# Kernel optimization log

Hardware: AMD Instinct MI355X
Metric: run time of the kernel (lower is better)

Reference implementation:

```python
import jax, jax.numpy as jnp
import numpy as np

N = 50000
E = 800000
DIM_IN = 128
DIM_H = 16
HEADS = 8
DIM_OUT = 16
NEG_SLOPE = 0.2


def setup_inputs() -> dict:
    key = jax.random.key(0)
    ks = jax.random.split(key, 12)
    def glorot(k, shape):
        fan_in = shape[0]
        return jax.random.normal(k, shape, dtype=jnp.float32) / np.sqrt(fan_in)
    x = jax.random.normal(ks[0], (N, DIM_IN), dtype=jnp.float32)
    edge_index = jax.random.randint(ks[1], (2, E), 0, N, dtype=jnp.int64)
    # layer 1: GATv2Conv(dim_in, dim_h, heads=8)
    Wl1 = glorot(ks[2], (DIM_IN, HEADS * DIM_H))
    Wr1 = glorot(ks[3], (DIM_IN, HEADS * DIM_H))
    att1 = glorot(ks[4], (HEADS, DIM_H))
    bias1 = jnp.zeros((HEADS * DIM_H,), dtype=jnp.float32)
    # layer 2: GATv2Conv(dim_h*heads, dim_out, heads=1)
    Wl2 = glorot(ks[5], (HEADS * DIM_H, DIM_OUT))
    Wr2 = glorot(ks[6], (HEADS * DIM_H, DIM_OUT))
    att2 = glorot(ks[7], (1, DIM_OUT))
    bias2 = jnp.zeros((DIM_OUT,), dtype=jnp.float32)
    return {"x": x, "edge_index": edge_index, "Wl1": Wl1, "Wr1": Wr1,
            "att1": att1, "bias1": bias1, "Wl2": Wl2, "Wr2": Wr2,
            "att2": att2, "bias2": bias2}


def gatv2_layer(x, src, dst, Wl, Wr, att, bias, n_nodes, heads, ch):
    # x: [N, F_in]; src/dst: [Etot] (self-loops included)
    xl = (x @ Wl).reshape(n_nodes, heads, ch)  # source transform
    xr = (x @ Wr).reshape(n_nodes, heads, ch)  # target transform
    e = jax.nn.leaky_relu(xl[src] + xr[dst], NEG_SLOPE)      # [Etot, H, C]
    logits = jnp.einsum('ehc,hc->eh', e, att)                # [Etot, H]
    # segment softmax over incoming edges of each target node
    m = jax.ops.segment_max(logits, dst, num_segments=n_nodes)
    a = jnp.exp(logits - m[dst])
    denom = jax.ops.segment_sum(a, dst, num_segments=n_nodes)
    alpha = a / denom[dst]                                   # [Etot, H]
    out = jax.ops.segment_sum(xl[src] * alpha[:, :, None], dst,
                              num_segments=n_nodes)          # [N, H, C]
    return out.reshape(n_nodes, heads * ch) + bias


def reference(x, edge_index, Wl1, Wr1, att1, bias1, Wl2, Wr2, att2, bias2):
    # PyG GATv2Conv adds self-loops by default
    loops = jnp.arange(N, dtype=edge_index.dtype)
    src = jnp.concatenate([edge_index[0], loops])
    dst = jnp.concatenate([edge_index[1], loops])
    # dropout is identity in eval mode
    h = gatv2_layer(x, src, dst, Wl1, Wr1, att1, bias1, N, HEADS, DIM_H)
    h = jax.nn.elu(h)
    h = gatv2_layer(h, src, dst, Wl2, Wr2, att2, bias2, N, 1, DIM_OUT)
    return h, jax.nn.log_softmax(h, axis=1)
```

## Files before the change

kernel.cpp:

```cpp
#include <hip/hip_runtime.h>
#include <hip/hip_bf16.h>
#include <math.h>

#define NN 50000
#define EE 800000
#define DIN 128
#define HEADS 8
#define DH 16
#define DOUT 16
#define NEG 0.2f
#define GM 32
#define GB ((NN + GM - 1) / GM)
#define NB ((NN + 255) / 256)
#define DEGB ((EE / 4 + 255) / 256)
#define PAD 64

typedef __attribute__((ext_vector_type(8))) short bf16x8;
typedef __attribute__((ext_vector_type(4))) float f32x4;

__device__ __forceinline__ unsigned pack2bf(float a, float b) {
    union { __hip_bfloat162 h; unsigned u; } c;
    c.h = __float22bfloat162_rn(make_float2(a, b));
    return c.u;
}
__device__ __forceinline__ unsigned short f2bf(float v) {
    union { __hip_bfloat16 h; unsigned short u; } c;
    c.h = __float2bfloat16(v);
    return c.u;
}
__device__ __forceinline__ float bflo(unsigned u) { return __uint_as_float(u << 16); }
__device__ __forceinline__ float bfhi(unsigned u) { return __uint_as_float(u & 0xffff0000u); }

__global__ __launch_bounds__(256) void init_wcvt(int* __restrict__ cnt,
                                                 int* __restrict__ esrcPad,
                                                 const float* __restrict__ Wl,
                                                 const float* __restrict__ Wr,
                                                 unsigned short* __restrict__ Wb) {
    int b = blockIdx.x, t = threadIdx.x;
    if (b < NB) {
        int i = b * 256 + t;
        if (i < NN) {
            cnt[i] = 1;
            esrcPad[(size_t)i * PAD] = i;
        }
    } else {
        int i = (b - NB) * 256 + t;
        int n = i >> 7, k = i & 127;
        float v = (n < 128) ? Wl[k * 128 + n] : Wr[k * 128 + (n - 128)];
        Wb[i] = f2bf(v);
    }
}

__global__ __launch_bounds__(256) void fill_gemm1(const int* __restrict__ ei,
                                                  int* __restrict__ cnt,
                                                  int* __restrict__ esrcPad,
                                                  const float* __restrict__ x,
                                                  const unsigned short* __restrict__ Wb,
                                                  unsigned short* __restrict__ xlb,
                                                  float* __restrict__ xr) {
    __shared__ unsigned short As[GM][136];
    int t = threadIdx.x;
    if (blockIdx.x >= GB) {
        int i = (blockIdx.x - GB) * 256 + t;
        if (i >= EE / 4) return;
        int4 ss = ((const int4*)ei)[i];
        int4 dd = ((const int4*)(ei + EE))[i];
        int p;
        p = atomicAdd(&cnt[dd.x], 1); esrcPad[(size_t)dd.x * PAD + p] = ss.x;
        p = atomicAdd(&cnt[dd.y], 1); esrcPad[(size_t)dd.y * PAD + p] = ss.y;
        p = atomicAdd(&cnt[dd.z], 1); esrcPad[(size_t)dd.z * PAD + p] = ss.z;
        p = atomicAdd(&cnt[dd.w], 1); esrcPad[(size_t)dd.w * PAD + p] = ss.w;
        return;
    }
    int n0 = blockIdx.x * GM;
    {
        int row = t >> 3, seg = t & 7;
        int nsrc = n0 + row < NN ? n0 + row : NN - 1;
        const float4* xp = (const float4*)(x + (size_t)nsrc * DIN + 16 * seg);
        float4 v0 = xp[0], v1 = xp[1], v2 = xp[2], v3 = xp[3];
        uint4 p0 = make_uint4(pack2bf(v0.x, v0.y), pack2bf(v0.z, v0.w),
                              pack2bf(v1.x, v1.y), pack2bf(v1.z, v1.w));
        uint4 p1 = make_uint4(pack2bf(v2.x, v2.y), pack2bf(v2.z, v2.w),
                              pack2bf(v3.x, v3.y), pack2bf(v3.z, v3.w));
        *(uint4*)&As[row][16 * seg]     = p0;
        *(uint4*)&As[row][16 * seg + 8] = p1;
    }
    __syncthreads();
    int lane = t & 63, w = t >> 6;
    int m = lane & 15, quad = lane >> 4;
    f32x4 acc[2][4];
#pragma unroll
    for (int mt = 0; mt < 2; ++mt)
#pragma unroll
        for (int nt = 0; nt < 4; ++nt) acc[mt][nt] = (f32x4){0.f, 0.f, 0.f, 0.f};
#pragma unroll
    for (int ks = 0; ks < 4; ++ks) {
        int k = 32 * ks + 8 * quad;
        bf16x8 a0 = *(const bf16x8*)&As[m][k];
        bf16x8 a1 = *(const bf16x8*)&As[16 + m][k];
#pragma unroll
        for (int nt = 0; nt < 4; ++nt) {
            int n = 64 * w + 16 * nt + m;
            bf16x8 b = *(const bf16x8*)(Wb + (size_t)n * 128 + k);
            acc[0][nt] = __builtin_amdgcn_mfma_f32_16x16x32_bf16(a0, b, acc[0][nt], 0, 0, 0);
            acc[1][nt] = __builtin_amdgcn_mfma_f32_16x16x32_bf16(a1, b, acc[1][nt], 0, 0, 0);
        }
    }
#pragma unroll
    for (int mt = 0; mt < 2; ++mt) {
#pragma unroll
        for (int nt = 0; nt < 4; ++nt) {
            int col = 64 * w + 16 * nt + m;
            int rbase = n0 + 16 * mt + 4 * quad;
            if (col < 128) {
#pragma unroll
                for (int r = 0; r < 4; ++r) {
                    int row = rbase + r;
                    if (row < NN) xlb[(size_t)row * DIN + col] = f2bf(acc[mt][nt][r]);
                }
            } else {
#pragma unroll
                for (int r = 0; r < 4; ++r) {
                    int row = rbase + r;
                    if (row < NN) xr[(size_t)row * DIN + (col - 128)] = acc[mt][nt][r];
                }
            }
        }
    }
}

__global__ __launch_bounds__(256) void l1_fused(const int* __restrict__ esrcPad,
                                                const int* __restrict__ cnt,
                                                const unsigned short* __restrict__ xlb,
                                                const float* __restrict__ xr,
                                                const float* __restrict__ att,
                                                const float* __restrict__ bias,
                                                float* __restrict__ hout) {
    int d = blockIdx.x * 4 + (threadIdx.x >> 6);
    int lane = threadIdx.x & 63;
    int quarter = lane >> 4;
    int q16 = lane & 15;
    int rs = d * PAD;
    int re = rs + cnt[d];
    int last = re - 1;
    float4 xr0 = ((const float4*)(xr + (size_t)d * DIN))[2 * q16];
    float4 xr1 = ((const float4*)(xr + (size_t)d * DIN))[2 * q16 + 1];
    float4 at0 = ((const float4*)att)[2 * q16];
    float4 at1 = ((const float4*)att)[2 * q16 + 1];
    float4 a0 = make_float4(0.f, 0.f, 0.f, 0.f);
    float4 a1 = make_float4(0.f, 0.f, 0.f, 0.f);
    float l = 0.f;
    int slot = rs + quarter;
    int c0 = slot < last ? slot : last;
    int s0 = esrcPad[c0];
    int c1 = slot + 4 < last ? slot + 4 : last;
    int s1 = esrcPad[c1];
    uint4 row = ((const uint4*)(xlb + (size_t)s0 * DIN))[q16];
    for (; slot < re; slot += 4) {
        uint4 cur = row;
        int c2 = slot + 8 < last ? slot + 8 : last;
        int s2 = esrcPad[c2];
        row = ((const uint4*)(xlb + (size_t)s1 * DIN))[q16];
        s1 = s2;
        float f0 = bflo(cur.x), f1 = bfhi(cur.x);
        float f2 = bflo(cur.y), f3 = bfhi(cur.y);
        float f4 = bflo(cur.z), f5 = bfhi(cur.z);
        float f6 = bflo(cur.w), f7 = bfhi(cur.w);
        float v0 = f0 + xr0.x; v0 = fmaxf(v0, NEG * v0);
        float v1 = f1 + xr0.y; v1 = fmaxf(v1, NEG * v1);
        float v2 = f2 + xr0.z; v2 = fmaxf(v2, NEG * v2);
        float v3 = f3 + xr0.w; v3 = fmaxf(v3, NEG * v3);
        float v4 = f4 + xr1.x; v4 = fmaxf(v4, NEG * v4);
        float v5 = f5 + xr1.y; v5 = fmaxf(v5, NEG * v5);
        float v6 = f6 + xr1.z; v6 = fmaxf(v6, NEG * v6);
        float v7 = f7 + xr1.w; v7 = fmaxf(v7, NEG * v7);
        float w = at0.x * v0 + at0.y * v1 + at0.z * v2 + at0.w * v3
                + at1.x * v4 + at1.y * v5 + at1.z * v6 + at1.w * v7;
        w += __shfl_xor(w, 1);
        float p = __expf(w);
        a0.x += p * f0; a0.y += p * f1; a0.z += p * f2; a0.w += p * f3;
        a1.x += p * f4; a1.y += p * f5; a1.z += p * f6; a1.w += p * f7;
        l += p;
    }
#pragma unroll
    for (int off = 16; off < 64; off <<= 1) {
        a0.x += __shfl_xor(a0.x, off); a0.y += __shfl_xor(a0.y, off);
        a0.z += __shfl_xor(a0.z, off); a0.w += __shfl_xor(a0.w, off);
        a1.x += __shfl_xor(a1.x, off); a1.y += __shfl_xor(a1.y, off);
        a1.z += __shfl_xor(a1.z, off); a1.w += __shfl_xor(a1.w, off);
        l += __shfl_xor(l, off);
    }
    if (quarter == 0) {
        float inv = 1.f / l;
        float4 b0 = ((const float4*)bias)[2 * q16];
        float4 b1 = ((const float4*)bias)[2 * q16 + 1];
        float4 o0, o1;
        o0.x = a0.x * inv + b0.x; o0.x = o0.x > 0.f ? o0.x : expm1f(o0.x);
        o0.y = a0.y * inv + b0.y; o0.y = o0.y > 0.f ? o0.y : expm1f(o0.y);
        o0.z = a0.z * inv + b0.z; o0.z = o0.z > 0.f ? o0.z : expm1f(o0.z);
        o0.w = a0.w * inv + b0.w; o0.w = o0.w > 0.f ? o0.w : expm1f(o0.w);
        o1.x = a1.x * inv + b1.x; o1.x = o1.x > 0.f ? o1.x : expm1f(o1.x);
        o1.y = a1.y * inv + b1.y; o1.y = o1.y > 0.f ? o1.y : expm1f(o1.y);
        o1.z = a1.z * inv + b1.z; o1.z = o1.z > 0.f ? o1.z : expm1f(o1.z);
        o1.w = a1.w * inv + b1.w; o1.w = o1.w > 0.f ? o1.w : expm1f(o1.w);
        ((float4*)(hout + (size_t)d * DIN))[2 * q16]     = o0;
        ((float4*)(hout + (size_t)d * DIN))[2 * q16 + 1] = o1;
    }
}

__global__ __launch_bounds__(256) void gemm2(const float* __restrict__ h,
                                             const float* __restrict__ Wl,
                                             const float* __restrict__ Wr,
                                             float* __restrict__ xl, float* __restrict__ xr) {
    __shared__ float xs[GM][DIN + 4];
    int t = threadIdx.x;
    int n0 = blockIdx.x * GM;
    {
        int r = t >> 3, q0 = t & 7;
        int n = n0 + r;
        float4* dstq = (float4*)(xs[r]);
        if (n < NN) {
            const float4* src = (const float4*)(h + (size_t)n * DIN);
#pragma unroll
            for (int k = 0; k < 4; ++k) dstq[q0 + 8 * k] = src[q0 + 8 * k];
        } else {
#pragma unroll
            for (int k = 0; k < 4; ++k) dstq[q0 + 8 * k] = make_float4(0.f, 0.f, 0.f, 0.f);
        }
    }
    __syncthreads();
    int q = t & 7;
    int g = t >> 3;
    const float* __restrict__ W = (q < 4) ? Wl : Wr;
    int cq = q & 3;
    float4 acc = make_float4(0.f, 0.f, 0.f, 0.f);
#pragma unroll 8
    for (int i = 0; i < DIN; ++i) {
        float4 w = ((const float4*)(W + (size_t)i * DOUT))[cq];
        float xv = xs[g][i];
        acc.x += xv * w.x; acc.y += xv * w.y; acc.z += xv * w.z; acc.w += xv * w.w;
    }
    int n = n0 + g;
    if (n < NN) {
        float* __restrict__ dst = (q < 4) ? xl : xr;
        ((float4*)(dst + (size_t)n * DOUT))[cq] = acc;
    }
}

__global__ __launch_bounds__(256) void l2_fused(const int* __restrict__ esrcPad,
                                                const int* __restrict__ cnt,
                                                const float* __restrict__ xl,
                                                const float* __restrict__ xr,
                                                const float* __restrict__ att,
                                                const float* __restrict__ bias,
                                                float* __restrict__ out) {
    int d = blockIdx.x * 4 + (threadIdx.x >> 6);
    int lane = threadIdx.x & 63;
    int sl = lane >> 2;
    int q = lane & 3;
    int rs = d * PAD;
    int re = rs + cnt[d];
    int last = re - 1;
    float4 xrq = ((const float4*)(xr + (size_t)d * DOUT))[q];
    float4 atq = ((const float4*)att)[q];
    float4 acc = make_float4(0.f, 0.f, 0.f, 0.f);
    float l = 0.f;
    int slot = rs + sl;
    int c0 = slot < last ? slot : last;
    int s0 = esrcPad[c0];
    for (; slot < re; slot += 16) {
        int c1 = slot + 16 < last ? slot + 16 : last;
        int s1 = esrcPad[c1];
        float4 cur = ((const float4*)(xl + (size_t)s0 * DOUT))[q];
        s0 = s1;
        float v0 = cur.x + xrq.x; v0 = fmaxf(v0, NEG * v0);
        float v1 = cur.y + xrq.y; v1 = fmaxf(v1, NEG * v1);
        float v2 = cur.z + xrq.z; v2 = fmaxf(v2, NEG * v2);
        float v3 = cur.w + xrq.w; v3 = fmaxf(v3, NEG * v3);
        float w = atq.x * v0 + atq.y * v1 + atq.z * v2 + atq.w * v3;
        w += __shfl_xor(w, 1);
        w += __shfl_xor(w, 2);
        float p = __expf(w);
        acc.x += p * cur.x; acc.y += p * cur.y;
        acc.z += p * cur.z; acc.w += p * cur.w;
        l += p;
    }
#pragma unroll
    for (int off = 4; off < 64; off <<= 1) {
        acc.x += __shfl_xor(acc.x, off);
        acc.y += __shfl_xor(acc.y, off);
        acc.z += __shfl_xor(acc.z, off);
        acc.w += __shfl_xor(acc.w, off);
        l += __shfl_xor(l, off);
    }
    float inv = 1.f / l;
    float4 b = ((const float4*)bias)[q];
    float4 v;
    v.x = acc.x * inv + b.x; v.y = acc.y * inv + b.y;
    v.z = acc.z * inv + b.z; v.w = acc.w * inv + b.w;
    float m = fmaxf(fmaxf(v.x, v.y), fmaxf(v.z, v.w));
    m = fmaxf(m, __shfl_xor(m, 1));
    m = fmaxf(m, __shfl_xor(m, 2));
    float es = __expf(v.x - m) + __expf(v.y - m) + __expf(v.z - m) + __expf(v.w - m);
    es += __shfl_xor(es, 1);
    es += __shfl_xor(es, 2);
    float lse = m + __logf(es);
    if (sl == 0) {
        ((float4*)(out + (size_t)d * DOUT))[q] = v;
        float4 ls;
        ls.x = v.x - lse; ls.y = v.y - lse; ls.z = v.z - lse; ls.w = v.w - lse;
        ((float4*)(out + (size_t)NN * DOUT + (size_t)d * DOUT))[q] = ls;
    }
}

extern "C" void kernel_launch(void* const* d_in, const int* in_sizes, int n_in,
                              void* d_out, int out_size, void* d_ws, size_t ws_size,
                              hipStream_t stream) {
    const float* x     = (const float*)d_in[0];
    const int*   ei    = (const int*)d_in[1];
    const float* Wl1   = (const float*)d_in[2];
    const float* Wr1   = (const float*)d_in[3];
    const float* att1  = (const float*)d_in[4];
    const float* bias1 = (const float*)d_in[5];
    const float* Wl2   = (const float*)d_in[6];
    const float* Wr2   = (const float*)d_in[7];
    const float* att2  = (const float*)d_in[8];
    const float* bias2 = (const float*)d_in[9];
    float* out = (float*)d_out;

    float* xr1    = (float*)d_ws;
    float* hout   = xr1 + (size_t)NN * DIN;
    float* xl2    = hout + (size_t)NN * DIN;
    float* xr2    = xl2 + (size_t)NN * DOUT;
    unsigned short* xlb = (unsigned short*)(xr2 + (size_t)NN * DOUT);
    unsigned short* Wb  = xlb + (size_t)NN * DIN;
    int*   esrcPad = (int*)(Wb + 256 * 128);
    int*   cnt    = esrcPad + (size_t)NN * PAD;

    const int B = 256;
    init_wcvt<<<NB + 128, B, 0, stream>>>(cnt, esrcPad, Wl1, Wr1, Wb);
    fill_gemm1<<<GB + DEGB, B, 0, stream>>>(ei, cnt, esrcPad, x, Wb, xlb, xr1);

    l1_fused<<<NN / 4, B, 0, stream>>>(esrcPad, cnt, xlb, xr1, att1, bias1, hout);

    gemm2<<<(NN + GM - 1) / GM, B, 0, stream>>>(hout, Wl2, Wr2, xl2, xr2);

    l2_fused<<<NN / 4, B, 0, stream>>>(esrcPad, cnt, xl2, xr2, att2, bias2, out);
}
```

Baseline: 257.0 us.

## Store layer-1 output in bf16 and run gemm2 on MFMA

Layer-1 output h is now written as packed bf16 instead of fp32, and gemm2 is rewritten to use MFMA 16x16x32 bf16 with a pre-converted bf16 copy of Wl2/Wr2 built in the init kernel. This halves the h write/read traffic and replaces the scalar FMA loop with matrix instructions. The edge-fill blocks are also moved before the GEMM blocks in fill_gemm1 so atomics start earlier. Reduced precision of h adds some rounding error to layer 2 inputs.

```diff
diff --git a/kernel.cpp b/kernel.cpp
--- a/kernel.cpp
+++ b/kernel.cpp
@@ -35,7 +35,10 @@
                                                  int* __restrict__ esrcPad,
                                                  const float* __restrict__ Wl,
                                                  const float* __restrict__ Wr,
-                                                 unsigned short* __restrict__ Wb) {
+                                                 unsigned short* __restrict__ Wb,
+                                                 const float* __restrict__ Wl2,
+                                                 const float* __restrict__ Wr2,
+                                                 unsigned short* __restrict__ Wb2) {
     int b = blockIdx.x, t = threadIdx.x;
     if (b < NB) {
         int i = b * 256 + t;
@@ -43,11 +46,16 @@
             cnt[i] = 1;
             esrcPad[(size_t)i * PAD] = i;
         }
-    } else {
+    } else if (b < NB + 128) {
         int i = (b - NB) * 256 + t;
         int n = i >> 7, k = i & 127;
         float v = (n < 128) ? Wl[k * 128 + n] : Wr[k * 128 + (n - 128)];
         Wb[i] = f2bf(v);
+    } else {
+        int i = (b - NB - 128) * 256 + t;
+        int n = i >> 7, k = i & 127;
+        float v = (n < 16) ? Wl2[k * 16 + n] : Wr2[k * 16 + (n - 16)];
+        Wb2[i] = f2bf(v);
     }
 }
 
@@ -60,8 +68,8 @@
                                                   float* __restrict__ xr) {
     __shared__ unsigned short As[GM][136];
     int t = threadIdx.x;
-    if (blockIdx.x >= GB) {
-        int i = (blockIdx.x - GB) * 256 + t;
+    if (blockIdx.x < DEGB) {
+        int i = blockIdx.x * 256 + t;
         if (i >= EE / 4) return;
         int4 ss = ((const int4*)ei)[i];
         int4 dd = ((const int4*)(ei + EE))[i];
@@ -72,7 +80,7 @@
         p = atomicAdd(&cnt[dd.w], 1); esrcPad[(size_t)dd.w * PAD + p] = ss.w;
         return;
     }
-    int n0 = blockIdx.x * GM;
+    int n0 = (blockIdx.x - DEGB) * GM;
     {
         int row = t >> 3, seg = t & 7;
         int nsrc = n0 + row < NN ? n0 + row : NN - 1;
@@ -135,7 +143,7 @@
                                                 const float* __restrict__ xr,
                                                 const float* __restrict__ att,
                                                 const float* __restrict__ bias,
-                                                float* __restrict__ hout) {
+                                                unsigned short* __restrict__ hb) {
     int d = blockIdx.x * 4 + (threadIdx.x >> 6);
     int lane = threadIdx.x & 63;
     int quarter = lane >> 4;
@@ -203,47 +211,42 @@
         o1.y = a1.y * inv + b1.y; o1.y = o1.y > 0.f ? o1.y : expm1f(o1.y);
         o1.z = a1.z * inv + b1.z; o1.z = o1.z > 0.f ? o1.z : expm1f(o1.z);
         o1.w = a1.w * inv + b1.w; o1.w = o1.w > 0.f ? o1.w : expm1f(o1.w);
-        ((float4*)(hout + (size_t)d * DIN))[2 * q16]     = o0;
-        ((float4*)(hout + (size_t)d * DIN))[2 * q16 + 1] = o1;
-    }
-}
-
-__global__ __launch_bounds__(256) void gemm2(const float* __restrict__ h,
-                                             const float* __restrict__ Wl,
-                                             const float* __restrict__ Wr,
-                                             float* __restrict__ xl, float* __restrict__ xr) {
-    __shared__ float xs[GM][DIN + 4];
+        uint4 pk = make_uint4(pack2bf(o0.x, o0.y), pack2bf(o0.z, o0.w),
+                              pack2bf(o1.x, o1.y), pack2bf(o1.z, o1.w));
+        ((uint4*)(hb + (size_t)d * DIN))[q16] = pk;
+    }
+}
+
+__global__ __launch_bounds__(256) void gemm2(const unsigned short* __restrict__ hb,
+                                             const unsigned short* __restrict__ Wb2,
+                                             float* __restrict__ xl2, float* __restrict__ xr2) {
+    __shared__ unsigned short As[GM][136];
     int t = threadIdx.x;
     int n0 = blockIdx.x * GM;
     {
-        int r = t >> 3, q0 = t & 7;
-        int n = n0 + r;
-        float4* dstq = (float4*)(xs[r]);
-        if (n < NN) {
-            const float4* src = (const float4*)(h + (size_t)n * DIN);
-#pragma unroll
-            for (int k = 0; k < 4; ++k) dstq[q0 + 8 * k] = src[q0 + 8 * k];
-        } else {
-#pragma unroll
-            for (int k = 0; k < 4; ++k) dstq[q0 + 8 * k] = make_float4(0.f, 0.f, 0.f, 0.f);
-        }
+        int row = t >> 3, s8 = t & 7;
+        int nsrc = n0 + row < NN ? n0 + row : NN - 1;
+        const uint4* src = (const uint4*)(hb + (size_t)nsrc * DIN);
+        *(uint4*)&As[row][8 * s8]      = src[s8];
+        *(uint4*)&As[row][8 * s8 + 64] = src[s8 + 8];
     }
     __syncthreads();
-    int q = t & 7;
-    int g = t >> 3;
-    const float* __restrict__ W = (q < 4) ? Wl : Wr;
-    int cq = q & 3;
-    float4 acc = make_float4(0.f, 0.f, 0.f, 0.f);
-#pragma unroll 8
-    for (int i = 0; i < DIN; ++i) {
-        float4 w = ((const float4*)(W + (size_t)i * DOUT))[cq];
-        float xv = xs[g][i];
-        acc.x += xv * w.x; acc.y += xv * w.y; acc.z += xv * w.z; acc.w += xv * w.w;
-    }
-    int n = n0 + g;
-    if (n < NN) {
-        float* __restrict__ dst = (q < 4) ? xl : xr;
-        ((float4*)(dst + (size_t)n * DOUT))[cq] = acc;
+    int lane = t & 63, w = t >> 6;
+    int m = lane & 15, quad = lane >> 4;
+    int mt = w & 1, nt = w >> 1;
+    f32x4 acc = (f32x4){0.f, 0.f, 0.f, 0.f};
+#pragma unroll
+    for (int ks = 0; ks < 4; ++ks) {
+        int k = 32 * ks + 8 * quad;
+        bf16x8 a = *(const bf16x8*)&As[16 * mt + m][k];
+        bf16x8 b = *(const bf16x8*)(Wb2 + (size_t)(16 * nt + m) * 128 + k);
+        acc = __builtin_amdgcn_mfma_f32_16x16x32_bf16(a, b, acc, 0, 0, 0);
+    }
+    float* __restrict__ dst = (nt == 0) ? xl2 : xr2;
+#pragma unroll
+    for (int r = 0; r < 4; ++r) {
+        int node = n0 + 16 * mt + 4 * quad + r;
+        if (node < NN) dst[(size_t)node * DOUT + m] = acc[r];
     }
 }
 
@@ -329,21 +332,22 @@
     float* out = (float*)d_out;
 
     float* xr1    = (float*)d_ws;
-    float* hout   = xr1 + (size_t)NN * DIN;
-    float* xl2    = hout + (size_t)NN * DIN;
+    float* xl2    = xr1 + (size_t)NN * DIN;
     float* xr2    = xl2 + (size_t)NN * DOUT;
     unsigned short* xlb = (unsigned short*)(xr2 + (size_t)NN * DOUT);
-    unsigned short* Wb  = xlb + (size_t)NN * DIN;
-    int*   esrcPad = (int*)(Wb + 256 * 128);
+    unsigned short* hb  = xlb + (size_t)NN * DIN;
+    unsigned short* Wb  = hb + (size_t)NN * DIN;
+    unsigned short* Wb2 = Wb + 256 * 128;
+    int*   esrcPad = (int*)(Wb2 + 32 * 128);
     int*   cnt    = esrcPad + (size_t)NN * PAD;
 
     const int B = 256;
-    init_wcvt<<<NB + 128, B, 0, stream>>>(cnt, esrcPad, Wl1, Wr1, Wb);
-    fill_gemm1<<<GB + DEGB, B, 0, stream>>>(ei, cnt, esrcPad, x, Wb, xlb, xr1);
-
-    l1_fused<<<NN / 4, B, 0, stream>>>(esrcPad, cnt, xlb, xr1, att1, bias1, hout);
-
-    gemm2<<<(NN + GM - 1) / GM, B, 0, stream>>>(hout, Wl2, Wr2, xl2, xr2);
+    init_wcvt<<<NB + 144, B, 0, stream>>>(cnt, esrcPad, Wl1, Wr1, Wb, Wl2, Wr2, Wb2);
+    fill_gemm1<<<DEGB + GB, B, 0, stream>>>(ei, cnt, esrcPad, x, Wb, xlb, xr1);
+
+    l1_fused<<<NN / 4, B, 0, stream>>>(esrcPad, cnt, xlb, xr1, att1, bias1, hb);
+
+    gemm2<<<GB, B, 0, stream>>>(hb, Wb2, xl2, xr2);
 
     l2_fused<<<NN / 4, B, 0, stream>>>(esrcPad, cnt, xl2, xr2, att2, bias2, out);
 }
```

Result: faster. 231.3 us (-10.0%).
